# Kernel tuning notes

Measured on AMD Instinct MI355X. Metric: run time of the kernel, lower is better.

The kernel has to match this reference:

```python
import jax, jax.numpy as jnp
import numpy as np

N_X, N_U, N_Y, HID, T = 1024, 512, 128, 4096, 8192


def setup_inputs() -> dict:
    key = jax.random.key(0)
    ks = jax.random.split(key, 6)
    s = lambda fan_in: 1.0 / np.sqrt(fan_in)
    return {
        "x0": jax.random.normal(ks[0], (N_X,), jnp.float32),
        "u": jax.random.normal(ks[1], (T, N_U), jnp.float32),
        "f_w1": jax.random.normal(ks[2], (N_X + N_U, HID), jnp.float32) * s(N_X + N_U),
        "f_b1": jnp.zeros((HID,), jnp.float32),
        "f_w2": jax.random.normal(ks[3], (HID, N_X), jnp.float32) * s(HID),
        "f_b2": jnp.zeros((N_X,), jnp.float32),
        "g_w1": jax.random.normal(ks[4], (N_X, HID), jnp.float32) * s(N_X),
        "g_b1": jnp.zeros((HID,), jnp.float32),
        "g_w2": jax.random.normal(ks[5], (HID, N_Y), jnp.float32) * s(HID),
        "g_b2": jnp.zeros((N_Y,), jnp.float32),
    }


def reference(x0, u, f_w1, f_b1, f_w2, f_b2, g_w1, g_b1, g_w2, g_b2):
    # Simulator: scan over time; each step:
    #   xu = concat(x, u_t); new_x = f_xu(xu); y_t = g_x(x)
    def step(x, u_t):
        xu = jnp.concatenate([x, u_t])                       # [n_x + n_u]
        new_x = jnp.tanh(xu @ f_w1 + f_b1) @ f_w2 + f_b2     # [n_x]
        y_t = jnp.tanh(x @ g_w1 + g_b1) @ g_w2 + g_b2        # [n_y]
        return new_x, y_t

    _, y = jax.lax.scan(step, x0, u)                         # y: [T, n_y]
    return y
```

## Files before the change

### kernel.cpp

```cpp
#include <hip/hip_runtime.h>
#include <hip/hip_bf16.h>
#include <stdint.h>

#define T_STEPS 8192
#define NX 1024
#define NU 512
#define NY 128
#define HID 4096

#define SEQ_WGS 256
#define SEQ_BLK 512

typedef __attribute__((ext_vector_type(8))) short bf16x8;
typedef __attribute__((ext_vector_type(4))) float f32x4;

__device__ __forceinline__ float bf2f(ushort u) {
  union { uint32_t i; float f; } v; v.i = ((uint32_t)u) << 16; return v.f;
}
__device__ __forceinline__ ushort f2bf(float f) {
  union { float f; uint32_t i; } v; v.f = f;
  uint32_t r = v.i + 0x7fffu + ((v.i >> 16) & 1u);
  return (ushort)(r >> 16);
}
__device__ __forceinline__ float lof(uint32_t u) {
  union { uint32_t i; float f; } v; v.i = u << 16; return v.f;
}
__device__ __forceinline__ float hif(uint32_t u) {
  union { uint32_t i; float f; } v; v.i = u & 0xffff0000u; return v.f;
}


__global__ void cvt_bf16_kernel(const float* __restrict__ in, ushort* __restrict__ out, int n) {
  int i = blockIdx.x * blockDim.x + threadIdx.x;
  int stride = gridDim.x * blockDim.x;
  for (; i < n; i += stride) out[i] = f2bf(in[i]);
}

__global__ void transpose_cvt_kernel(const float* __restrict__ in, ushort* __restrict__ out,
                                     int R, int C) {
  __shared__ float tile[32][33];
  int bx = blockIdx.x, by = blockIdx.y;
  int tx = threadIdx.x, ty = threadIdx.y;
#pragma unroll
  for (int yy = 0; yy < 4; ++yy) {
    long r = (long)by * 32 + ty + yy * 8;
    long c = (long)bx * 32 + tx;
    tile[ty + yy * 8][tx] = in[r * C + c];
  }
  __syncthreads();
#pragma unroll
  for (int yy = 0; yy < 4; ++yy) {
    long c = (long)bx * 32 + ty + yy * 8;
    long r = (long)by * 32 + tx;
    out[c * R + r] = f2bf(tile[tx][ty + yy * 8]);
  }
}

__global__ void bias_dh_kernel(const float* __restrict__ fw1, const float* __restrict__ fb1,
                               const float* __restrict__ fb2, float* __restrict__ biasDH) {
  int j = blockIdx.x * blockDim.x + threadIdx.x;
  float s = fb1[j];
  for (int k = 0; k < NX; ++k) s += fb2[k] * fw1[(long)k * HID + j];
  biasDH[j] = s;
}

__global__ void fixup_row0_kernel(const float* __restrict__ fw1, const float* __restrict__ fb1,
                                  const float* __restrict__ u, const float* __restrict__ x0,
                                  ushort* __restrict__ DH, uint32_t* __restrict__ htag) {
  int j = blockIdx.x * blockDim.x + threadIdx.x;
  float s = fb1[j];
  for (int k = 0; k < NU; ++k) s += u[k] * fw1[(long)(NX + k) * HID + j];
  for (int k = 0; k < NX; ++k) s += x0[k] * fw1[(long)k * HID + j];
  float h = tanhf(s);
  ushort hb = f2bf(h);
  DH[j] = hb;
  htag[j] = ((uint32_t)hb << 16);
}

__global__ void x0_row_kernel(const float* __restrict__ x0, ushort* __restrict__ X) {
  int j = blockIdx.x * blockDim.x + threadIdx.x;
  if (j < NX) X[j] = f2bf(x0[j]);
}

#define GBM 128
#define GBN 128
#define GBK 32
#define LDT 40

__global__ __launch_bounds__(256) void gemm_kernel(
    const ushort* __restrict__ A, const ushort* __restrict__ BT,
    void* __restrict__ Cout, const float* __restrict__ bias,
    int M, int N, int K, int flags)
{
  __shared__ ushort Al[GBM * LDT];
  __shared__ ushort Bl[GBN * LDT];
  const int tid = threadIdx.x;
  const int bm = blockIdx.y, bn = blockIdx.x;
  const int wave = tid >> 6, lane = tid & 63;
  const int wr = wave >> 1, wc = wave & 1;
  const int l15 = lane & 15, l4 = lane >> 4;

  f32x4 acc[4][4];
#pragma unroll
  for (int m = 0; m < 4; ++m)
#pragma unroll
    for (int n = 0; n < 4; ++n) acc[m][n] = (f32x4){0.f, 0.f, 0.f, 0.f};

  const int r_t = tid >> 1;
  const int h_t = (tid & 1) * 16;
  const long arow = (long)bm * GBM + r_t;
  const long brow = (long)bn * GBN + r_t;

  for (int k0 = 0; k0 < K; k0 += GBK) {
    uint4 a0 = make_uint4(0,0,0,0), a1 = make_uint4(0,0,0,0);
    if (arow < M) {
      const ushort* p = A + arow * K + k0 + h_t;
      a0 = *(const uint4*)p;
      a1 = *(const uint4*)(p + 8);
    }
    const ushort* q = BT + brow * K + k0 + h_t;
    uint4 b0 = *(const uint4*)q;
    uint4 b1 = *(const uint4*)(q + 8);
    __syncthreads();
    *(uint4*)&Al[r_t * LDT + h_t]     = a0;
    *(uint4*)&Al[r_t * LDT + h_t + 8] = a1;
    *(uint4*)&Bl[r_t * LDT + h_t]     = b0;
    *(uint4*)&Bl[r_t * LDT + h_t + 8] = b1;
    __syncthreads();

    bf16x8 af[4], bfv[4];
#pragma unroll
    for (int m = 0; m < 4; ++m)
      af[m] = *(const bf16x8*)&Al[(wr * 64 + m * 16 + l15) * LDT + l4 * 8];
#pragma unroll
    for (int n = 0; n < 4; ++n)
      bfv[n] = *(const bf16x8*)&Bl[(wc * 64 + n * 16 + l15) * LDT + l4 * 8];
#pragma unroll
    for (int m = 0; m < 4; ++m)
#pragma unroll
      for (int n = 0; n < 4; ++n)
        acc[m][n] = __builtin_amdgcn_mfma_f32_16x16x32_bf16(af[m], bfv[n], acc[m][n], 0, 0, 0);
  }

  const bool f32out = (flags & 2) != 0;
  const bool dotanh = (flags & 1) != 0;
#pragma unroll
  for (int m = 0; m < 4; ++m) {
#pragma unroll
    for (int n = 0; n < 4; ++n) {
#pragma unroll
      for (int j = 0; j < 4; ++j) {
        long grow = (long)bm * GBM + wr * 64 + m * 16 + l4 * 4 + j;
        int  gcol = bn * GBN + wc * 64 + n * 16 + l15;
        if (grow < M) {
          float v = acc[m][n][j];
          if (bias) v += bias[gcol];
          if (dotanh) v = tanhf(v);
          if (f32out) ((float*)Cout)[grow * N + gcol] = v;
          else        ((ushort*)Cout)[grow * N + gcol] = f2bf(v);
        }
      }
    }
  }
}

__global__ __launch_bounds__(SEQ_BLK, 2) void seq_kernel(
    const ushort* __restrict__ MT, ushort* __restrict__ DH,
    uint32_t* __restrict__ htag, int nsteps)
{
  __shared__ ushort hl[HID];
  const int tid = threadIdx.x;
  const int w = blockIdx.x;
  const int col = tid >> 5;
  const int ksub = tid & 31;
  const int gcol = (w << 4) + col;

  float4 mreg[32];
  {
    const uint4* mrow = (const uint4*)(MT + (size_t)gcol * HID);
#pragma unroll
    for (int j = 0; j < 16; ++j) {
      uint4 m = mrow[ksub + 32 * j];
      mreg[2 * j]     = make_float4(lof(m.x), hif(m.x), lof(m.y), hif(m.y));
      mreg[2 * j + 1] = make_float4(lof(m.z), hif(m.z), lof(m.w), hif(m.w));
    }
  }

  const bool prod = (ksub == 0);

  for (int i = 0; i < nsteps; ++i) {
    float dnext = 0.f;
    if (prod) dnext = bf2f(DH[(size_t)(i + 1) * HID + gcol]);

    {
      uint32_t* slot = htag + (size_t)(i & 1) * HID;
      const uint32_t target = (uint32_t)i & 0xffffu;
      uint32_t x[8];
      bool pend[8];
#pragma unroll
      for (int j = 0; j < 8; ++j) pend[j] = true;
      int rem = 8;
      while (rem) {
#pragma unroll
        for (int j = 0; j < 8; ++j)
          if (pend[j])
            x[j] = __hip_atomic_load(&slot[tid + 512 * j], __ATOMIC_RELAXED,
                                     __HIP_MEMORY_SCOPE_AGENT);
#pragma unroll
        for (int j = 0; j < 8; ++j)
          if (pend[j] && (x[j] & 0xffffu) == target) { pend[j] = false; --rem; }
        if (rem) __builtin_amdgcn_s_sleep(1);
      }
#pragma unroll
      for (int j = 0; j < 8; ++j) hl[tid + 512 * j] = (ushort)(x[j] >> 16);
    }
    __syncthreads();

    float a0 = 0.f, a1 = 0.f, a2 = 0.f, a3 = 0.f;
    const ushort* hp = hl + ksub * 8;
#pragma unroll
    for (int j = 0; j < 16; ++j) {
      uint4 hv = *(const uint4*)(hp + 256 * j);
      float4 m0 = mreg[2 * j], m1 = mreg[2 * j + 1];
      a0 = fmaf(m0.x, lof(hv.x), a0);
      a1 = fmaf(m0.y, hif(hv.x), a1);
      a2 = fmaf(m0.z, lof(hv.y), a2);
      a3 = fmaf(m0.w, hif(hv.y), a3);
      a0 = fmaf(m1.x, lof(hv.z), a0);
      a1 = fmaf(m1.y, hif(hv.z), a1);
      a2 = fmaf(m1.z, lof(hv.w), a2);
      a3 = fmaf(m1.w, hif(hv.w), a3);
    }
    float acc = (a0 + a1) + (a2 + a3);
#pragma unroll
    for (int off = 16; off >= 1; off >>= 1)
      acc += __shfl_xor(acc, off, 64);

    if (prod) {
      float h = tanhf(acc + dnext);
      ushort hb = f2bf(h);
      uint32_t word = ((uint32_t)hb << 16) | ((uint32_t)(i + 1) & 0xffffu);
      __hip_atomic_store(htag + (size_t)((i + 1) & 1) * HID + gcol, word,
                         __ATOMIC_RELAXED, __HIP_MEMORY_SCOPE_AGENT);
      DH[(size_t)(i + 1) * HID + gcol] = hb;
    }
    __syncthreads();
  }
}


extern "C" void kernel_launch(void* const* d_in, const int* in_sizes, int n_in,
                              void* d_out, int out_size, void* d_ws, size_t ws_size,
                              hipStream_t stream) {
  const float* x0  = (const float*)d_in[0];
  const float* u   = (const float*)d_in[1];
  const float* fw1 = (const float*)d_in[2];
  const float* fb1 = (const float*)d_in[3];
  const float* fw2 = (const float*)d_in[4];
  const float* fb2 = (const float*)d_in[5];
  const float* gw1 = (const float*)d_in[6];
  const float* gb1 = (const float*)d_in[7];
  const float* gw2 = (const float*)d_in[8];
  const float* gb2 = (const float*)d_in[9];
  float* out = (float*)d_out;

  char* ws = (char*)d_ws;
  size_t off = 0;
  auto alloc = [&](size_t bytes) -> char* {
    char* p = ws + off; off += (bytes + 255) & ~(size_t)255; return p;
  };
  ushort* MT     = (ushort*)alloc((size_t)HID * HID * 2);
  ushort* DH     = (ushort*)alloc((size_t)T_STEPS * HID * 2);
  ushort* X      = (ushort*)alloc((size_t)T_STEPS * NX * 2);
  ushort* W1xT   = (ushort*)alloc((size_t)HID * NX * 2);
  ushort* W1uT   = (ushort*)alloc((size_t)HID * NU * 2);
  ushort* W2bf   = (ushort*)alloc((size_t)HID * NX * 2);
  ushort* W2T    = (ushort*)alloc((size_t)NX * HID * 2);
  ushort* Gw1T   = (ushort*)alloc((size_t)HID * NX * 2);
  ushort* Gw2T   = (ushort*)alloc((size_t)NY * HID * 2);
  ushort* Ubf    = (ushort*)alloc((size_t)T_STEPS * NU * 2);
  float*  biasDH = (float*)alloc((size_t)HID * 4);
  uint32_t* htag = (uint32_t*)alloc((size_t)2 * HID * 4);
  if (off > ws_size) return;

  cvt_bf16_kernel<<<2048, 256, 0, stream>>>(u, Ubf, T_STEPS * NU);
  cvt_bf16_kernel<<<2048, 256, 0, stream>>>(fw2, W2bf, HID * NX);
  transpose_cvt_kernel<<<dim3(HID/32, NX/32), dim3(32, 8), 0, stream>>>(fw1, W1xT, NX, HID);
  transpose_cvt_kernel<<<dim3(HID/32, NU/32), dim3(32, 8), 0, stream>>>(fw1 + (size_t)NX * HID, W1uT, NU, HID);
  transpose_cvt_kernel<<<dim3(NX/32, HID/32), dim3(32, 8), 0, stream>>>(fw2, W2T, HID, NX);
  transpose_cvt_kernel<<<dim3(HID/32, NX/32), dim3(32, 8), 0, stream>>>(gw1, Gw1T, NX, HID);
  transpose_cvt_kernel<<<dim3(NY/32, HID/32), dim3(32, 8), 0, stream>>>(gw2, Gw2T, HID, NY);
  bias_dh_kernel<<<HID/256, 256, 0, stream>>>(fw1, fb1, fb2, biasDH);

  gemm_kernel<<<dim3(HID/128, HID/128), 256, 0, stream>>>(W1xT, W2bf, MT, nullptr, HID, HID, NX, 0);
  gemm_kernel<<<dim3(HID/128, T_STEPS/128), 256, 0, stream>>>(Ubf, W1uT, DH, biasDH, T_STEPS, HID, NU, 0);
  fixup_row0_kernel<<<HID/256, 256, 0, stream>>>(fw1, fb1, u, x0, DH, htag);

  {
    int nsteps = T_STEPS - 2;
    void* MT_p = (void*)MT; void* DH_p = (void*)DH; void* ht_p = (void*)htag;
    void* args[] = { &MT_p, &DH_p, &ht_p, &nsteps };
    hipError_t e = hipLaunchCooperativeKernel((const void*)seq_kernel, dim3(SEQ_WGS),
                                              dim3(SEQ_BLK), args, 0, stream);
    if (e != hipSuccess) {
      (void)hipGetLastError();
      seq_kernel<<<SEQ_WGS, SEQ_BLK, 0, stream>>>(MT, DH, htag, nsteps);
    }
  }

  x0_row_kernel<<<NX/256, 256, 0, stream>>>(x0, X);
  gemm_kernel<<<dim3(NX/128, T_STEPS/128), 256, 0, stream>>>(DH, W2T, X + NX, fb2, T_STEPS - 1, NX, HID, 0);
  gemm_kernel<<<dim3(HID/128, T_STEPS/128), 256, 0, stream>>>(X, Gw1T, DH, gb1, T_STEPS, HID, NX, 1);
  gemm_kernel<<<dim3(NY/128, T_STEPS/128), 256, 0, stream>>>(DH, Gw2T, out, gb2, T_STEPS, NY, HID, 2);
}
```

Baseline: 19.66 ms.

## Pack two columns per wave with bf16 dot2 and 64-bit tagged polling

Each wave now computes two output columns, keeping the weights as packed bf16 in registers and accumulating with the bf16 fdot2 instruction instead of unpacked fp32 FMAs. The flag/value words are written and polled as 64-bit pairs, so each thread polls four contiguous words in one loop rather than eight scattered words. The trailing barrier is dropped and an extra barrier is added after staging h into LDS. Launch bounds move to one block per CU. The aim is to cut polling traffic, register footprint and ALU work per step in the latency-bound recurrence, at the cost of fewer parallel reduction lanes per column and a changed synchronisation structure.

```diff
diff --git a/kernel.cpp b/kernel.cpp
--- a/kernel.cpp
+++ b/kernel.cpp
@@ -13,6 +13,7 @@
 
 typedef __attribute__((ext_vector_type(8))) short bf16x8;
 typedef __attribute__((ext_vector_type(4))) float f32x4;
+typedef __attribute__((ext_vector_type(2))) short s16x2;
 
 __device__ __forceinline__ float bf2f(ushort u) {
   union { uint32_t i; float f; } v; v.i = ((uint32_t)u) << 16; return v.f;
@@ -27,6 +28,16 @@
 }
 __device__ __forceinline__ float hif(uint32_t u) {
   union { uint32_t i; float f; } v; v.i = u & 0xffff0000u; return v.f;
+}
+
+__device__ __forceinline__ float dot2bf(uint32_t h, uint32_t m, float acc) {
+#if __has_builtin(__builtin_amdgcn_fdot2_f32_bf16)
+  return __builtin_amdgcn_fdot2_f32_bf16(__builtin_bit_cast(s16x2, h),
+                                         __builtin_bit_cast(s16x2, m), acc, false);
+#else
+  acc = fmaf(lof(h), lof(m), acc);
+  return fmaf(hif(h), hif(m), acc);
+#endif
 }
 
 
@@ -164,87 +175,94 @@
   }
 }
 
-__global__ __launch_bounds__(SEQ_BLK, 2) void seq_kernel(
+__global__ __launch_bounds__(SEQ_BLK, 1) void seq_kernel(
     const ushort* __restrict__ MT, ushort* __restrict__ DH,
     uint32_t* __restrict__ htag, int nsteps)
 {
   __shared__ ushort hl[HID];
   const int tid = threadIdx.x;
-  const int w = blockIdx.x;
-  const int col = tid >> 5;
-  const int ksub = tid & 31;
-  const int gcol = (w << 4) + col;
-
-  float4 mreg[32];
+  const int w = threadIdx.x >> 6;
+  const int lane = tid & 63;
+  const int c0 = (blockIdx.x << 4) + (w << 1);
+
+  uint4 mA[8], mB[8];
   {
-    const uint4* mrow = (const uint4*)(MT + (size_t)gcol * HID);
-#pragma unroll
-    for (int j = 0; j < 16; ++j) {
-      uint4 m = mrow[ksub + 32 * j];
-      mreg[2 * j]     = make_float4(lof(m.x), hif(m.x), lof(m.y), hif(m.y));
-      mreg[2 * j + 1] = make_float4(lof(m.z), hif(m.z), lof(m.w), hif(m.w));
-    }
-  }
-
-  const bool prod = (ksub == 0);
+    const uint4* rA = (const uint4*)(MT + (size_t)c0 * HID);
+    const uint4* rB = (const uint4*)(MT + (size_t)(c0 + 1) * HID);
+#pragma unroll
+    for (int j = 0; j < 8; ++j) {
+      mA[j] = rA[lane + 64 * j];
+      mB[j] = rB[lane + 64 * j];
+    }
+  }
+
+  const bool prod = (lane == 0);
+  unsigned long long* tagbase = (unsigned long long*)htag;
 
   for (int i = 0; i < nsteps; ++i) {
-    float dnext = 0.f;
-    if (prod) dnext = bf2f(DH[(size_t)(i + 1) * HID + gcol]);
-
+    float dA = 0.f, dB = 0.f;
+    if (prod) {
+      uint32_t dw = *(const uint32_t*)(DH + (size_t)(i + 1) * HID + c0);
+      dA = lof(dw); dB = hif(dw);
+    }
+
+    unsigned long long x0, x1, x2, x3;
     {
-      uint32_t* slot = htag + (size_t)(i & 1) * HID;
-      const uint32_t target = (uint32_t)i & 0xffffu;
-      uint32_t x[8];
-      bool pend[8];
-#pragma unroll
-      for (int j = 0; j < 8; ++j) pend[j] = true;
-      int rem = 8;
-      while (rem) {
-#pragma unroll
-        for (int j = 0; j < 8; ++j)
-          if (pend[j])
-            x[j] = __hip_atomic_load(&slot[tid + 512 * j], __ATOMIC_RELAXED,
-                                     __HIP_MEMORY_SCOPE_AGENT);
-#pragma unroll
-        for (int j = 0; j < 8; ++j)
-          if (pend[j] && (x[j] & 0xffffu) == target) { pend[j] = false; --rem; }
-        if (rem) __builtin_amdgcn_s_sleep(1);
+      unsigned long long* slot = tagbase + (size_t)(i & 1) * (HID / 2) + (tid << 2);
+      const uint32_t tg = (uint32_t)i & 0xffffu;
+      for (;;) {
+        x0 = __hip_atomic_load(slot + 0, __ATOMIC_RELAXED, __HIP_MEMORY_SCOPE_AGENT);
+        x1 = __hip_atomic_load(slot + 1, __ATOMIC_RELAXED, __HIP_MEMORY_SCOPE_AGENT);
+        x2 = __hip_atomic_load(slot + 2, __ATOMIC_RELAXED, __HIP_MEMORY_SCOPE_AGENT);
+        x3 = __hip_atomic_load(slot + 3, __ATOMIC_RELAXED, __HIP_MEMORY_SCOPE_AGENT);
+        uint32_t bad = (((uint32_t)x0 ^ tg) | ((uint32_t)x1 ^ tg) |
+                        ((uint32_t)x2 ^ tg) | ((uint32_t)x3 ^ tg)) & 0xffffu;
+        if (bad == 0) break;
+        __builtin_amdgcn_s_sleep(1);
       }
-#pragma unroll
-      for (int j = 0; j < 8; ++j) hl[tid + 512 * j] = (ushort)(x[j] >> 16);
     }
     __syncthreads();
-
-    float a0 = 0.f, a1 = 0.f, a2 = 0.f, a3 = 0.f;
-    const ushort* hp = hl + ksub * 8;
-#pragma unroll
-    for (int j = 0; j < 16; ++j) {
-      uint4 hv = *(const uint4*)(hp + 256 * j);
-      float4 m0 = mreg[2 * j], m1 = mreg[2 * j + 1];
-      a0 = fmaf(m0.x, lof(hv.x), a0);
-      a1 = fmaf(m0.y, hif(hv.x), a1);
-      a2 = fmaf(m0.z, lof(hv.y), a2);
-      a3 = fmaf(m0.w, hif(hv.y), a3);
-      a0 = fmaf(m1.x, lof(hv.z), a0);
-      a1 = fmaf(m1.y, hif(hv.z), a1);
-      a2 = fmaf(m1.z, lof(hv.w), a2);
-      a3 = fmaf(m1.w, hif(hv.w), a3);
-    }
-    float acc = (a0 + a1) + (a2 + a3);
-#pragma unroll
-    for (int off = 16; off >= 1; off >>= 1)
-      acc += __shfl_xor(acc, off, 64);
+    {
+      uint4 p;
+      p.x = ((uint32_t)(x0 >> 16) & 0xffffu) | ((uint32_t)(x0 >> 32) & 0xffff0000u);
+      p.y = ((uint32_t)(x1 >> 16) & 0xffffu) | ((uint32_t)(x1 >> 32) & 0xffff0000u);
+      p.z = ((uint32_t)(x2 >> 16) & 0xffffu) | ((uint32_t)(x2 >> 32) & 0xffff0000u);
+      p.w = ((uint32_t)(x3 >> 16) & 0xffffu) | ((uint32_t)(x3 >> 32) & 0xffff0000u);
+      ((uint4*)hl)[tid] = p;
+    }
+    __syncthreads();
+
+    float accA = 0.f, accB = 0.f;
+    const uint4* h4 = (const uint4*)hl;
+#pragma unroll
+    for (int j = 0; j < 8; ++j) {
+      uint4 hv = h4[lane + 64 * j];
+      accA = dot2bf(hv.x, mA[j].x, accA);
+      accB = dot2bf(hv.x, mB[j].x, accB);
+      accA = dot2bf(hv.y, mA[j].y, accA);
+      accB = dot2bf(hv.y, mB[j].y, accB);
+      accA = dot2bf(hv.z, mA[j].z, accA);
+      accB = dot2bf(hv.z, mB[j].z, accB);
+      accA = dot2bf(hv.w, mA[j].w, accA);
+      accB = dot2bf(hv.w, mB[j].w, accB);
+    }
+#pragma unroll
+    for (int off = 32; off >= 1; off >>= 1) {
+      accA += __shfl_xor(accA, off, 64);
+      accB += __shfl_xor(accB, off, 64);
+    }
 
     if (prod) {
-      float h = tanhf(acc + dnext);
-      ushort hb = f2bf(h);
-      uint32_t word = ((uint32_t)hb << 16) | ((uint32_t)(i + 1) & 0xffffu);
-      __hip_atomic_store(htag + (size_t)((i + 1) & 1) * HID + gcol, word,
+      ushort ha = f2bf(tanhf(accA + dA));
+      ushort hb = f2bf(tanhf(accB + dB));
+      uint32_t tg1 = (uint32_t)(i + 1) & 0xffffu;
+      unsigned long long word =
+          ((unsigned long long)(((uint32_t)hb << 16) | tg1) << 32) |
+          (unsigned long long)(((uint32_t)ha << 16) | tg1);
+      __hip_atomic_store(tagbase + (size_t)((i + 1) & 1) * (HID / 2) + (c0 >> 1), word,
                          __ATOMIC_RELAXED, __HIP_MEMORY_SCOPE_AGENT);
-      DH[(size_t)(i + 1) * HID + gcol] = hb;
-    }
-    __syncthreads();
+      *(uint32_t*)(DH + (size_t)(i + 1) * HID + c0) = (uint32_t)ha | ((uint32_t)hb << 16);
+    }
   }
 }
 
```

Measured after the change: 23.35 ms. 18.8% more time.
